# Optimization experiments

Hardware: AMD Instinct MI355X
Metric: run time of the kernel (lower is better)

Reference implementation:

```python
import jax, jax.numpy as jnp
from jax import lax
import numpy as np

ALPHA = 0.5   # init alpha
TEMP = 0.1    # init temp (used in nt_xent_loss)
TEMP2 = 0.05  # hardcoded temperature inside nt_xent_loss2
EPS = 1e-12

N, D, C = 4096, 128, 20


def setup_inputs() -> dict:
    key = jax.random.key(0)
    k1, k2, k3 = jax.random.split(key, 3)
    cls_feats = jax.random.normal(k1, (N, D), dtype=jnp.float32)
    predicts = jax.random.normal(k2, (N, C), dtype=jnp.float32)
    targets = jax.random.randint(k3, (N,), 0, C)
    return {"cls_feats": cls_feats, "predicts": predicts, "targets": targets}


def _forward(cls_feats, predicts, targets):
    n = cls_feats.shape[0]
    # F.normalize(dim=-1): x / max(||x||, eps)
    norms = jnp.maximum(jnp.linalg.norm(cls_feats, axis=-1, keepdims=True), EPS)
    feats = cls_feats / norms

    # --- cross entropy (mean reduction) ---
    logp_cls = jax.nn.log_softmax(predicts, axis=-1)
    ce_loss = -jnp.mean(jnp.take_along_axis(logp_cls, targets[:, None], axis=1))

    same = (targets[:, None] == targets[None, :]).astype(feats.dtype)  # [N,N]
    diff = 1.0 - same

    # --- nt_xent_loss (supervised contrastive, mask excludes diagonal) ---
    mask = same * (1.0 - jnp.eye(n, dtype=feats.dtype))
    logits = jnp.matmul(feats, feats.T) / TEMP
    logits = logits - lax.stop_gradient(jnp.max(logits, axis=1, keepdims=True))
    exp_logits = jnp.exp(logits) * mask
    log_prob = logits - jnp.log(jnp.sum(exp_logits, axis=1, keepdims=True) + EPS)
    mask_sum = jnp.sum(mask, axis=1)
    mask_sum = jnp.where(mask_sum == 0, 1.0, mask_sum)
    cl_loss = -jnp.mean(jnp.sum(mask * log_prob, axis=1) / mask_sum)

    # --- nt_xent_loss2, vectorized ---
    # In the torch loop, negtive_indices always equals arange(N) (same-label
    # indices include i; union with diff-label indices covers everything).
    # Row j of the per-i masked matrix is: zeros if label[j]==label[i], else
    # D2[j,:]*diff[j,:] (independent of i). A zero row contributes N to the
    # stabilized exp-sum; masked zeros contribute exp(-rowmax) entries, which
    # the single precomputation below reproduces exactly.
    D2 = jnp.matmul(feats, feats.T) / TEMP2
    B = D2 * diff                                  # [N,N]
    r = jnp.sum(jnp.exp(B - jnp.max(B, axis=1, keepdims=True)), axis=1)  # [N]
    c = jnp.sum(diff, axis=1)                      # diff-label count per row
    n_same = jnp.sum(same, axis=1)
    S = jnp.matmul(diff, r) + n_same * n           # sum over all rows j of exp-sums
    S = jnp.where(c > 0, S, 0.0)                   # 'continue' when no diff label
    negsum = jnp.matmul(diff, c)                   # ((1-same_rows)*diff).sum() per i
    all_zero = jnp.all(negsum == 0)
    x = jnp.where(all_zero, S, S / jnp.where(negsum == 0, 1.0, negsum))
    logp = -jnp.log(x + EPS)                       # per-row scalar
    ms2 = jnp.sum(same, axis=1)                    # >= 1 (includes self)
    pos_logits = jnp.sum(same * logp[:, None], axis=1) / ms2
    triple_loss = -jnp.mean(pos_logits)

    return (1.0 - ALPHA) * ce_loss + ALPHA * cl_loss + 0.5 * ALPHA * triple_loss


def reference(cls_feats, predicts, targets):
    return _forward(cls_feats, predicts, targets)
```

## Files before the change

kernel.cpp:

```cpp
#include <hip/hip_runtime.h>
#include <hip/hip_bf16.h>

#define NN 4096
#define DD 128
#define CC 20
#define NSPLIT 16
#define CPS (NN / NSPLIT)
#define ROWS_PER_WAVE 16
#define ROWS_PER_BLOCK 64
#define NSTRIP (NN / ROWS_PER_BLOCK)
#define BSTRIDE 152

typedef __attribute__((ext_vector_type(8))) short short8;
typedef __attribute__((ext_vector_type(4))) float floatx4;

__global__ void k_prep(const float* __restrict__ x, const float* __restrict__ pred,
                       const int* __restrict__ tgt,
                       __hip_bfloat16* __restrict__ feats,
                       float* __restrict__ statsz,
                       float* __restrict__ ce_part) {
    __shared__ float ce_w[4];
    int wave = threadIdx.x >> 6, lane = threadIdx.x & 63;
    int row = blockIdx.x * 4 + wave;
    if (threadIdx.x < 16) statsz[blockIdx.x * 16 + threadIdx.x] = 0.0f;
    const float* xr = x + (size_t)row * DD;
    float2 v = *(const float2*)(xr + lane * 2);
    float ss = v.x * v.x + v.y * v.y;
    #pragma unroll
    for (int m = 1; m <= 32; m <<= 1) ss += __shfl_xor(ss, m);
    float inv = 1.0f / fmaxf(sqrtf(ss), 1e-12f);
    __hip_bfloat162 h;
    h.x = __float2bfloat16(v.x * inv);
    h.y = __float2bfloat16(v.y * inv);
    *(__hip_bfloat162*)(feats + (size_t)row * DD + lane * 2) = h;
    float p = (lane < CC) ? pred[(size_t)row * CC + lane] : -__builtin_inff();
    float mx = p;
    #pragma unroll
    for (int m = 1; m <= 32; m <<= 1) mx = fmaxf(mx, __shfl_xor(mx, m));
    float e = (lane < CC) ? __expf(p - mx) : 0.0f;
    #pragma unroll
    for (int m = 1; m <= 32; m <<= 1) e += __shfl_xor(e, m);
    float ptg = __shfl(p, tgt[row]);
    if (lane == 0) ce_w[wave] = mx + logf(e) - ptg;
    __syncthreads();
    if (threadIdx.x == 0)
        ce_part[blockIdx.x] = ce_w[0] + ce_w[1] + ce_w[2] + ce_w[3];
}

__launch_bounds__(256, 4)
__global__ void k_gram_stats(const __hip_bfloat16* __restrict__ feats,
                             const int* __restrict__ tgt,
                             float* __restrict__ E1g, float* __restrict__ T1g,
                             float* __restrict__ E2g, float* __restrict__ M2g) {
    __shared__ __align__(16) unsigned short Bt[64 * BSTRIDE];
    int lane  = threadIdx.x & 63;
    int wave  = threadIdx.x >> 6;
    int strip = blockIdx.x & (NSTRIP - 1);
    int split = blockIdx.x >> 6;
    int rbase  = strip * ROWS_PER_BLOCK + wave * ROWS_PER_WAVE;
    int cbase0 = split * CPS;
    int lr = lane & 15, lk = lane >> 4;

    short8 afrag[4];
    const __hip_bfloat16* arow = feats + (size_t)(rbase + lr) * DD;
    #pragma unroll
    for (int kc = 0; kc < 4; ++kc)
        afrag[kc] = *(const short8*)(arow + kc * 32 + lk * 8);

    int rl[4], gr[4];
    #pragma unroll
    for (int q = 0; q < 4; ++q) { gr[q] = rbase + lk * 4 + q; rl[q] = tgt[gr[q]]; }

    float E1[4] = {0,0,0,0}, T1[4] = {0,0,0,0}, E2[4] = {0,0,0,0}, m2[4] = {0,0,0,0};

    for (int t = 0; t < CPS / 64; ++t) {
        int cbase = cbase0 + t * 64;
        #pragma unroll
        for (int i = 0; i < 4; ++i) {
            int idx = threadIdx.x + i * 256;
            int row = idx >> 4, ch = idx & 15;
            *(floatx4*)(&Bt[row * BSTRIDE + ch * 8]) =
                *(const floatx4*)(feats + (size_t)(cbase + row) * DD + ch * 8);
        }
        __syncthreads();
        #pragma unroll
        for (int sc = 0; sc < 4; ++sc) {
            floatx4 acc = {0.0f, 0.0f, 0.0f, 0.0f};
            #pragma unroll
            for (int kc = 0; kc < 4; ++kc) {
                short8 b = *(const short8*)(&Bt[(sc * 16 + lr) * BSTRIDE + kc * 32 + lk * 8]);
                acc = __builtin_amdgcn_mfma_f32_16x16x32_bf16(afrag[kc], b, acc, 0, 0, 0);
            }
            int gc   = cbase + sc * 16 + lr;
            int clab = tgt[gc];
            #pragma unroll
            for (int q = 0; q < 4; ++q) {
                float g  = acc[q];
                float l1 = g * 10.0f;
                float tv = __expf(l1 - 10.0f);
                bool same = (rl[q] == clab);
                bool v1   = same && (gr[q] != gc);
                E1[q] += v1 ? tv : 0.0f;
                T1[q] += v1 ? l1 : 0.0f;
                E2[q] += same ? 0.0f : tv * tv;
                m2[q] = fmaxf(m2[q], same ? 0.0f : l1 + l1);
            }
        }
        __syncthreads();
    }

    #pragma unroll
    for (int q = 0; q < 4; ++q) {
        float e1 = E1[q], t1 = T1[q], e2 = E2[q], mm = m2[q];
        #pragma unroll
        for (int m = 1; m <= 8; m <<= 1) {
            e1 += __shfl_xor(e1, m);
            t1 += __shfl_xor(t1, m);
            e2 += __shfl_xor(e2, m);
            mm = fmaxf(mm, __shfl_xor(mm, m));
        }
        if (lr == 0) {
            int r = gr[q];
            atomicAdd(&E1g[r], e1);
            atomicAdd(&T1g[r], t1);
            atomicAdd(&E2g[r], e2);
            atomicMax((int*)&M2g[r], __float_as_int(mm));
        }
    }
}

#define FT 256
__global__ void k_finalize(const int* __restrict__ tgt,
                           const float* __restrict__ E1g, const float* __restrict__ T1g,
                           const float* __restrict__ E2g, const float* __restrict__ M2g,
                           const float* __restrict__ ce_part, float* __restrict__ out) {
    __shared__ int   hist[CC];
    __shared__ float Rt[CC];
    __shared__ float red[FT];
    __shared__ float s_cl;
    int t = threadIdx.x;
    if (t < CC) { hist[t] = 0; Rt[t] = 0.0f; }
    __syncthreads();
    for (int r = t; r < NN; r += FT) atomicAdd(&hist[tgt[r]], 1);
    __syncthreads();

    float clsum = 0.0f;
    for (int r = t; r < NN; r += FT) {
        int tg = tgt[r];
        int h  = hist[tg];
        float c1 = (float)(h - 1);
        float e1 = E1g[r], t1 = T1g[r], e2 = E2g[r], m = M2g[r];
        if (c1 > 0.0f) clsum += (t1 - c1 * (10.0f + logf(e1))) / c1;
        float rj = (float)h * __expf(-m) + e2 * __expf(20.0f - m);
        atomicAdd(&Rt[tg], rj);
    }
    float cesum = 0.0f;
    for (int i = t; i < 1024; i += FT) cesum += ce_part[i];

    red[t] = clsum; __syncthreads();
    for (int off = FT / 2; off; off >>= 1) {
        if (t < off) red[t] += red[t + off];
        __syncthreads();
    }
    if (t == 0) s_cl = red[0];
    __syncthreads();
    red[t] = cesum; __syncthreads();
    for (int off = FT / 2; off; off >>= 1) {
        if (t < off) red[t] += red[t + off];
        __syncthreads();
    }
    if (t == 0) {
        float ce = red[0] / (float)NN;
        float cl = -s_cl / (float)NN;
        float Rtot = 0.0f;
        long long Ctot = 0;
        for (int k = 0; k < CC; ++k) {
            Rtot += Rt[k];
            Ctot += (long long)hist[k] * (NN - hist[k]);
        }
        bool all_zero = true;
        for (int k = 0; k < CC; ++k)
            if (hist[k] > 0 && (Ctot - (long long)hist[k] * (NN - hist[k])) != 0) all_zero = false;
        float trip = 0.0f;
        for (int k = 0; k < CC; ++k) {
            if (hist[k] == 0) continue;
            long long c = NN - hist[k];
            float S = (c > 0) ? (Rtot - Rt[k] + (float)hist[k] * (float)NN) : 0.0f;
            long long ns = Ctot - (long long)hist[k] * (NN - hist[k]);
            float x = all_zero ? S : S / (float)(ns == 0 ? 1 : ns);
            trip += (float)hist[k] * logf(x + 1e-12f);
        }
        float triple = trip / (float)NN;
        out[0] = 0.5f * ce + 0.5f * cl + 0.25f * triple;
    }
}

extern "C" void kernel_launch(void* const* d_in, const int* in_sizes, int n_in,
                              void* d_out, int out_size, void* d_ws, size_t ws_size,
                              hipStream_t stream) {
    const float* cls  = (const float*)d_in[0];
    const float* pred = (const float*)d_in[1];
    const int*   tgt  = (const int*)d_in[2];
    float* out = (float*)d_out;
    char* ws = (char*)d_ws;

    __hip_bfloat16* feats = (__hip_bfloat16*)ws;
    float* stats = (float*)(ws + 1048576);
    float* E1g = stats;
    float* T1g = stats + NN;
    float* E2g = stats + 2 * NN;
    float* M2g = stats + 3 * NN;
    float* ce_part = stats + 4 * NN;

    hipLaunchKernelGGL(k_prep, dim3(NN / 4), dim3(256), 0, stream,
                       cls, pred, tgt, feats, stats, ce_part);
    hipLaunchKernelGGL(k_gram_stats, dim3(NSTRIP * NSPLIT), dim3(256), 0, stream,
                       feats, tgt, E1g, T1g, E2g, M2g);
    hipLaunchKernelGGL(k_finalize, dim3(1), dim3(FT), 0, stream,
                       tgt, E1g, T1g, E2g, M2g, ce_part, out);
}
```

Before: 94.60 us.

## Fold per-row stat reduction into gram kernel via last-block-per-strip class binning

Each gram block bumps a per-strip completion counter. The last block to finish a strip reduces that strip's 64 rows into per-class bins (CL sums, log terms, and the R_t components) using global atomics. The single-block finalize then only reads 80 bin values instead of looping over 4096 rows and four stat arrays, which shortens the serial tail. This adds threadfences, an atomic counter, and contended atomics on 20 class bins, and the regrouped CL sum changes floating-point summation order.

Result: slower. 169.5 us (+79.2%).

```diff
diff --git a/kernel.cpp b/kernel.cpp
--- a/kernel.cpp
+++ b/kernel.cpp
@@ -18,11 +18,13 @@
                        const int* __restrict__ tgt,
                        __hip_bfloat16* __restrict__ feats,
                        float* __restrict__ statsz,
+                       int* __restrict__ ctrlz,
                        float* __restrict__ ce_part) {
     __shared__ float ce_w[4];
     int wave = threadIdx.x >> 6, lane = threadIdx.x & 63;
     int row = blockIdx.x * 4 + wave;
     if (threadIdx.x < 16) statsz[blockIdx.x * 16 + threadIdx.x] = 0.0f;
+    if (blockIdx.x == 0 && threadIdx.x < 144) ctrlz[threadIdx.x] = 0;
     const float* xr = x + (size_t)row * DD;
     float2 v = *(const float2*)(xr + lane * 2);
     float ss = v.x * v.x + v.y * v.y;
@@ -51,8 +53,10 @@
 __global__ void k_gram_stats(const __hip_bfloat16* __restrict__ feats,
                              const int* __restrict__ tgt,
                              float* __restrict__ E1g, float* __restrict__ T1g,
-                             float* __restrict__ E2g, float* __restrict__ M2g) {
+                             float* __restrict__ E2g, float* __restrict__ M2g,
+                             float* __restrict__ bins, int* __restrict__ done) {
     __shared__ __align__(16) unsigned short Bt[64 * BSTRIDE];
+    __shared__ int s_old;
     int lane  = threadIdx.x & 63;
     int wave  = threadIdx.x >> 6;
     int strip = blockIdx.x & (NSTRIP - 1);
@@ -127,57 +131,65 @@
             atomicMax((int*)&M2g[r], __float_as_int(mm));
         }
     }
+
+    __threadfence();
+    __syncthreads();
+    if (threadIdx.x == 0) s_old = atomicAdd(&done[strip], 1);
+    __syncthreads();
+    if (s_old == NSPLIT - 1 && threadIdx.x < ROWS_PER_BLOCK) {
+        __threadfence();
+        int r  = strip * ROWS_PER_BLOCK + threadIdx.x;
+        int tg = tgt[r];
+        float e1 = atomicAdd(&E1g[r], 0.0f);
+        float t1 = atomicAdd(&T1g[r], 0.0f);
+        float e2 = atomicAdd(&E2g[r], 0.0f);
+        float m  = __int_as_float(atomicMax((int*)&M2g[r], 0));
+        float* clT = bins;
+        float* clL = bins + CC;
+        float* RtA = bins + 2 * CC;
+        float* RtB = bins + 3 * CC;
+        atomicAdd(&clT[tg], t1);
+        atomicAdd(&clL[tg], 10.0f + logf(e1));
+        atomicAdd(&RtA[tg], __expf(-m));
+        atomicAdd(&RtB[tg], e2 * __expf(20.0f - m));
+    }
 }
 
 #define FT 256
 __global__ void k_finalize(const int* __restrict__ tgt,
-                           const float* __restrict__ E1g, const float* __restrict__ T1g,
-                           const float* __restrict__ E2g, const float* __restrict__ M2g,
+                           const float* __restrict__ bins,
                            const float* __restrict__ ce_part, float* __restrict__ out) {
     __shared__ int   hist[CC];
-    __shared__ float Rt[CC];
     __shared__ float red[FT];
-    __shared__ float s_cl;
     int t = threadIdx.x;
-    if (t < CC) { hist[t] = 0; Rt[t] = 0.0f; }
+    if (t < CC) hist[t] = 0;
     __syncthreads();
     for (int r = t; r < NN; r += FT) atomicAdd(&hist[tgt[r]], 1);
-    __syncthreads();
-
-    float clsum = 0.0f;
-    for (int r = t; r < NN; r += FT) {
-        int tg = tgt[r];
-        int h  = hist[tg];
-        float c1 = (float)(h - 1);
-        float e1 = E1g[r], t1 = T1g[r], e2 = E2g[r], m = M2g[r];
-        if (c1 > 0.0f) clsum += (t1 - c1 * (10.0f + logf(e1))) / c1;
-        float rj = (float)h * __expf(-m) + e2 * __expf(20.0f - m);
-        atomicAdd(&Rt[tg], rj);
-    }
     float cesum = 0.0f;
     for (int i = t; i < 1024; i += FT) cesum += ce_part[i];
-
-    red[t] = clsum; __syncthreads();
-    for (int off = FT / 2; off; off >>= 1) {
-        if (t < off) red[t] += red[t + off];
-        __syncthreads();
-    }
-    if (t == 0) s_cl = red[0];
-    __syncthreads();
     red[t] = cesum; __syncthreads();
     for (int off = FT / 2; off; off >>= 1) {
         if (t < off) red[t] += red[t + off];
         __syncthreads();
     }
     if (t == 0) {
+        const float* clT = bins;
+        const float* clL = bins + CC;
+        const float* RtA = bins + 2 * CC;
+        const float* RtB = bins + 3 * CC;
         float ce = red[0] / (float)NN;
-        float cl = -s_cl / (float)NN;
+        float clsum = 0.0f;
+        float Rt[CC];
         float Rtot = 0.0f;
         long long Ctot = 0;
         for (int k = 0; k < CC; ++k) {
+            int h = hist[k];
+            if (h > 1) clsum += clT[k] / (float)(h - 1) - clL[k];
+            Rt[k] = (float)h * RtA[k] + RtB[k];
             Rtot += Rt[k];
-            Ctot += (long long)hist[k] * (NN - hist[k]);
-        }
+            Ctot += (long long)h * (NN - h);
+        }
+        float cl = -clsum / (float)NN;
         bool all_zero = true;
         for (int k = 0; k < CC; ++k)
             if (hist[k] > 0 && (Ctot - (long long)hist[k] * (NN - hist[k])) != 0) all_zero = false;
@@ -211,11 +223,13 @@
     float* E2g = stats + 2 * NN;
     float* M2g = stats + 3 * NN;
     float* ce_part = stats + 4 * NN;
+    float* bins = ce_part + 1024;
+    int*   done = (int*)(bins + 4 * CC);
 
     hipLaunchKernelGGL(k_prep, dim3(NN / 4), dim3(256), 0, stream,
-                       cls, pred, tgt, feats, stats, ce_part);
+                       cls, pred, tgt, feats, stats, (int*)bins, ce_part);
     hipLaunchKernelGGL(k_gram_stats, dim3(NSTRIP * NSPLIT), dim3(256), 0, stream,
-                       feats, tgt, E1g, T1g, E2g, M2g);
+                       feats, tgt, E1g, T1g, E2g, M2g, bins, done);
     hipLaunchKernelGGL(k_finalize, dim3(1), dim3(FT), 0, stream,
-                       tgt, E1g, T1g, E2g, M2g, ce_part, out);
-}
+                       tgt, bins, ce_part, out);
+}
```
